# Kernel tuning notes

Measured on AMD Instinct MI355X. Metric: run time of the kernel, lower is better.

Reference implementation:

```python
import jax, jax.numpy as jnp
import numpy as np
from jax import lax

# Dims
HID = 2048          # hidden_size
DI = 4096           # d_inner = expand * hidden
NH = 64             # mamba heads
P = 64              # head dim
N = 128             # d_state
G = 1               # n_groups
K = 4               # conv kernel
IM = 8192           # MLP intermediate
BB, L = 2, 2048
EPS = 1e-5
CONV_DIM = DI + 2 * G * N            # 4352
D_IN_PROJ = 2 * DI + 2 * G * N + NH  # 8512


def rmsnorm(x, w, eps=EPS):
    v = jnp.mean(jnp.square(x), axis=-1, keepdims=True)
    return x * jax.lax.rsqrt(v + eps) * w


def setup_inputs() -> dict:
    key = jax.random.key(0)
    ks = jax.random.split(key, 16)
    s = 0.02
    return {
        "positions": jnp.broadcast_to(jnp.arange(L, dtype=jnp.int32), (BB, L)),
        "hidden_states": jax.random.normal(ks[0], (BB, L, HID), jnp.float32),
        "residual": jax.random.normal(ks[1], (BB, L, HID), jnp.float32),
        "in_proj_w": jax.random.normal(ks[2], (D_IN_PROJ, HID), jnp.float32) * s,
        "conv_w": jax.random.normal(ks[3], (CONV_DIM, K), jnp.float32) * 0.2,
        "conv_b": jax.random.normal(ks[4], (CONV_DIM,), jnp.float32) * 0.02,
        "A_log": jnp.log(jnp.arange(1, NH + 1, dtype=jnp.float32)),
        "D": jnp.ones((NH,), jnp.float32),
        "dt_bias": jax.random.uniform(ks[5], (NH,), jnp.float32, -4.0, -2.0),
        "mixer_norm_w": jnp.ones((DI,), jnp.float32),
        "out_proj_w": jax.random.normal(ks[6], (HID, DI), jnp.float32) * s,
        "input_ln_w": jnp.ones((HID,), jnp.float32),
        "pre_ff_ln_w": jnp.ones((HID,), jnp.float32),
        "gate_up_w": jax.random.normal(ks[7], (2 * IM, HID), jnp.float32) * s,
        "down_w": jax.random.normal(ks[8], (HID, IM), jnp.float32) * s,
    }


def reference(positions, hidden_states, residual, in_proj_w, conv_w, conv_b,
              A_log, D, dt_bias, mixer_norm_w, out_proj_w, input_ln_w,
              pre_ff_ln_w, gate_up_w, down_w):
    del positions  # not used by the mamba mixer math
    B_, Lq, _ = hidden_states.shape

    # --- input RMSNorm with fused residual add ---
    residual = hidden_states + residual
    hs = rmsnorm(residual, input_ln_w)

    # --- Mamba2 mixer ---
    proj = jnp.einsum('bld,ed->ble', hs, in_proj_w)   # [B,L,D_IN_PROJ]
    z = proj[..., :DI]
    xBC = proj[..., DI:DI + CONV_DIM]
    dt = proj[..., DI + CONV_DIM:]                    # [B,L,NH]

    # causal depthwise conv (kernel K) + SiLU
    xp = jnp.pad(xBC, ((0, 0), (K - 1, 0), (0, 0)))
    conv = conv_b
    for k in range(K):
        conv = conv + xp[:, k:k + Lq, :] * conv_w[:, k]
    xBC = jax.nn.silu(conv)

    x = xBC[..., :DI].reshape(B_, Lq, NH, P)
    Bm = xBC[..., DI:DI + G * N].reshape(B_, Lq, G, N)
    Cm = xBC[..., DI + G * N:].reshape(B_, Lq, G, N)
    rep = NH // G
    Bm = jnp.repeat(Bm, rep, axis=2)                  # [B,L,NH,N]
    Cm = jnp.repeat(Cm, rep, axis=2)

    dt = jax.nn.softplus(dt + dt_bias)                # [B,L,NH]
    A = -jnp.exp(A_log)                               # [NH]
    dA = jnp.exp(dt * A)                              # [B,L,NH]

    def step(h, inp):
        x_t, B_t, C_t, dA_t, dt_t = inp               # [B,NH,P],[B,NH,N],[B,NH,N],[B,NH],[B,NH]
        h = dA_t[..., None, None] * h + \
            (dt_t[..., None, None] * x_t[..., None]) * B_t[:, :, None, :]
        y = jnp.einsum('bhpn,bhn->bhp', h, C_t)
        return h, y

    xs = (x.transpose(1, 0, 2, 3), Bm.transpose(1, 0, 2, 3),
          Cm.transpose(1, 0, 2, 3), dA.transpose(1, 0, 2), dt.transpose(1, 0, 2))
    h0 = jnp.zeros((B_, NH, P, N), hidden_states.dtype)
    _, ys = lax.scan(step, h0, xs)                    # [L,B,NH,P]
    y = ys.transpose(1, 0, 2, 3) + D[None, None, :, None] * x
    y = y.reshape(B_, Lq, DI)

    # gated RMSNorm (Mixer2RMSNormGated, n_groups=1)
    y = y * jax.nn.silu(z)
    y = rmsnorm(y, mixer_norm_w)
    mamba_out = jnp.einsum('bld,hd->blh', y, out_proj_w)

    # --- pre-FF RMSNorm with fused residual add ---
    residual2 = mamba_out + residual
    hs2 = rmsnorm(residual2, pre_ff_ln_w)

    # --- gated MLP (SiluAndMul) ---
    gu = jnp.einsum('bld,ed->ble', hs2, gate_up_w)    # [B,L,2*IM]
    act = jax.nn.silu(gu[..., :IM]) * gu[..., IM:]
    out = jnp.einsum('bli,hi->blh', act, down_w)
    return out, residual2
```

## Files before the change

### kernel.cpp

```cpp
#include <hip/hip_runtime.h>

#define T_TOK 4096
#define HID   2048
#define DI    4096
#define NH    64
#define PDIM  64
#define NSTATE 128
#define IM    8192
#define LSEQ  2048
#define CONVD 4352
#define DPROJ 8512
#define DPADR 8704
#define QC    64
#define NCH   32

typedef __bf16 bf16x8 __attribute__((ext_vector_type(8)));
typedef float  f32x4  __attribute__((ext_vector_type(4)));

__device__ __forceinline__ unsigned short f2bf(float f) {
  unsigned u = __float_as_uint(f);
  u = (u + 0x7fffu + ((u >> 16) & 1u)) >> 16;
  return (unsigned short)u;
}
__device__ __forceinline__ float bf2f(unsigned short h) {
  return __uint_as_float(((unsigned)h) << 16);
}
__device__ __forceinline__ float siluf(float x) {
  return x / (1.f + __expf(-x));
}

#define GLL(gaddr, laddr) __builtin_amdgcn_global_load_lds( \
    (const __attribute__((address_space(1))) void*)(gaddr), \
    (__attribute__((address_space(3))) void*)(laddr), 16, 0, 0)

__global__ __launch_bounds__(256) void k_cvt(const float* __restrict__ src,
                                             unsigned short* __restrict__ dst, int n4) {
  int gid = blockIdx.x * 256 + threadIdx.x;
  if (gid >= n4) return;
  float4 v = *(const float4*)&src[(size_t)gid * 4];
  unsigned short* o = dst + (size_t)gid * 4;
  o[0] = f2bf(v.x); o[1] = f2bf(v.y); o[2] = f2bf(v.z); o[3] = f2bf(v.w);
}

__global__ __launch_bounds__(256) void k_cvt_inproj(const float* __restrict__ src,
                                                    unsigned short* __restrict__ dst) {
  int gid = blockIdx.x * 256 + threadIdx.x;
  size_t idx4 = (size_t)gid * 4;
  int r = (int)(idx4 >> 11);
  unsigned short* o = dst + idx4;
  if (r < DPROJ) {
    float4 v = *(const float4*)&src[(size_t)r * HID + (idx4 & 2047)];
    o[0] = f2bf(v.x); o[1] = f2bf(v.y); o[2] = f2bf(v.z); o[3] = f2bf(v.w);
  } else {
    o[0] = 0; o[1] = 0; o[2] = 0; o[3] = 0;
  }
}

__global__ __launch_bounds__(256) void k_cvt_gu(const float* __restrict__ src,
                                                unsigned short* __restrict__ dst) {
  int gid = blockIdx.x * 256 + threadIdx.x;
  size_t idx4 = (size_t)gid * 4;
  int r = (int)(idx4 >> 11), k = (int)(idx4 & 2047);
  int g = r >> 6, j = r & 63;
  int srcr = (j < 32) ? (g * 32 + j) : (IM + g * 32 + (j - 32));
  float4 v = *(const float4*)&src[(size_t)srcr * HID + k];
  unsigned short* o = dst + idx4;
  o[0] = f2bf(v.x); o[1] = f2bf(v.y); o[2] = f2bf(v.z); o[3] = f2bf(v.w);
}

template <int EPI>
__global__ __launch_bounds__(512, 2)
void gemm8(const unsigned short* __restrict__ A, const unsigned short* __restrict__ W,
           int K, int ntn, int ldo, void* __restrict__ outp,
           const float* __restrict__ resid) {
  __shared__ __align__(16) char smem[131072];
  const int t = threadIdx.x;
  const int w = t >> 6, l = t & 63;
  const int lr = l & 15, hi = l >> 4;
  const int wr = w >> 2, wc = w & 3;

  const int q = (int)gridDim.x >> 3;
  const int bid = blockIdx.x;
  const int id2 = (bid & 7) * q + (bid >> 3);
  const int tn = id2 >> 4, tm = id2 & 15;
  const int m0b = tm << 8, n0b = tn << 8;

  const int srow = t >> 3;
  const int scole = ((t & 7) << 3) ^ ((t & 32) ? 16 : 0) ^ ((t & 64) ? 32 : 0);
  const unsigned short* Ag = A + (size_t)(m0b + srow) * K + scole;
  const unsigned short* Wg = W + (size_t)(n0b + srow) * K + scole;
  const int ldsw = w * 1024;

  const int fa = ((lr & 4) ? 32 : 0) | ((lr & 8) ? 64 : 0);
  const int arow = (wr * 128 + lr) * 128 + hi * 16;
  const int brow = (wc * 64 + lr) * 128 + hi * 16;
  const int aoffk[2] = {arow ^ fa, (arow + 64) ^ fa};
  const int boffk[2] = {brow ^ fa, (brow + 64) ^ fa};

#define ISSUE_A(jt, hh, bb) do { int p_ = (hh) * 2;                                   \
    GLL(Ag + (size_t)(p_ * 64) * K + (jt) * 64,                                       \
        smem + (bb) * 65536 + p_ * 8192 + ldsw);                                      \
    GLL(Ag + (size_t)(p_ * 64 + 64) * K + (jt) * 64,                                  \
        smem + (bb) * 65536 + p_ * 8192 + 8192 + ldsw); } while (0)
#define ISSUE_B(jt, hh, bb) do { int p_ = (hh) * 2;                                   \
    GLL(Wg + (size_t)(p_ * 64) * K + (jt) * 64,                                       \
        smem + (bb) * 65536 + 32768 + p_ * 8192 + ldsw);                              \
    GLL(Wg + (size_t)(p_ * 64 + 64) * K + (jt) * 64,                                  \
        smem + (bb) * 65536 + 32768 + p_ * 8192 + 8192 + ldsw); } while (0)

  f32x4 acc[8][4];
#pragma unroll
  for (int m = 0; m < 8; m++)
#pragma unroll
    for (int n = 0; n < 4; n++) acc[m][n] = (f32x4){0.f, 0.f, 0.f, 0.f};

  const int nkt = K >> 6;
  ISSUE_A(0, 0, 0); ISSUE_A(0, 1, 0);
  ISSUE_B(0, 0, 0); ISSUE_B(0, 1, 0);
  ISSUE_A(1, 0, 1); ISSUE_A(1, 1, 1);
  asm volatile("s_waitcnt vmcnt(4)" ::: "memory");
  __builtin_amdgcn_s_barrier();

#define CLUSTER(m0_) do {                                                             \
    __builtin_amdgcn_s_setprio(1);                                                    \
    _Pragma("unroll")                                                                 \
    for (int m = m0_; m < m0_ + 2; m++)                                               \
      _Pragma("unroll")                                                               \
      for (int n = 0; n < 4; n++)                                                     \
        _Pragma("unroll")                                                             \
        for (int kk = 0; kk < 2; kk++)                                                \
          acc[m][n] = __builtin_amdgcn_mfma_f32_16x16x32_bf16(afr[m][kk], bfr[n][kk], \
                                                              acc[m][n], 0, 0, 0);    \
    __builtin_amdgcn_s_setprio(0); } while (0)

  for (int j = 0; j < nkt; ++j) {
    const int cur = j & 1, nxt = cur ^ 1;
    const char* Ab = smem + cur * 65536;
    const char* Bb = Ab + 32768;
    if (j + 1 < nkt) { ISSUE_B(j + 1, 0, nxt); ISSUE_B(j + 1, 1, nxt); }
    bf16x8 bfr[4][2], afr[8][2];
#pragma unroll
    for (int n = 0; n < 4; n++)
#pragma unroll
      for (int kk = 0; kk < 2; kk++)
        bfr[n][kk] = *(const bf16x8*)(Bb + boffk[kk] + n * 2048);
#pragma unroll
    for (int m = 0; m < 8; m++)
#pragma unroll
      for (int kk = 0; kk < 2; kk++)
        afr[m][kk] = *(const bf16x8*)(Ab + aoffk[kk] + m * 2048);
    __builtin_amdgcn_s_barrier();
    CLUSTER(0);
    __builtin_amdgcn_s_barrier();
    if (j + 2 < nkt) ISSUE_A(j + 2, 0, cur);
    CLUSTER(2);
    __builtin_amdgcn_s_barrier();
    if (j + 2 < nkt) ISSUE_A(j + 2, 1, cur);
    CLUSTER(4);
    __builtin_amdgcn_s_barrier();
    CLUSTER(6);
    if (j + 2 < nkt) { asm volatile("s_waitcnt vmcnt(4)" ::: "memory"); }
    else             { asm volatile("s_waitcnt vmcnt(0)" ::: "memory"); }
    __builtin_amdgcn_s_barrier();
  }

  if constexpr (EPI == 0) {
    unsigned short* op = (unsigned short*)outp;
#pragma unroll
    for (int m = 0; m < 8; m++)
#pragma unroll
      for (int n = 0; n < 4; n++)
#pragma unroll
        for (int r = 0; r < 4; r++) {
          int row = m0b + wr * 128 + m * 16 + hi * 4 + r;
          int col = n0b + wc * 64 + n * 16 + lr;
          op[(size_t)row * ldo + col] = f2bf(acc[m][n][r]);
        }
  } else if constexpr (EPI == 2) {
    unsigned short* op = (unsigned short*)outp;
    const int gbase = (n0b + wc * 64) >> 1;
#pragma unroll
    for (int m = 0; m < 8; m++)
#pragma unroll
      for (int n = 0; n < 2; n++)
#pragma unroll
        for (int r = 0; r < 4; r++) {
          int row = m0b + wr * 128 + m * 16 + hi * 4 + r;
          int col = gbase + n * 16 + lr;
          float g = acc[m][n][r], u = acc[m][n + 2][r];
          op[(size_t)row * ldo + col] = f2bf(siluf(g) * u);
        }
  } else {
    float* op = (float*)outp;
#pragma unroll
    for (int m = 0; m < 8; m++)
#pragma unroll
      for (int n = 0; n < 4; n++)
#pragma unroll
        for (int r = 0; r < 4; r++) {
          int row = m0b + wr * 128 + m * 16 + hi * 4 + r;
          int col = n0b + wc * 64 + n * 16 + lr;
          float v = acc[m][n][r];
          if constexpr (EPI == 1) v += resid[(size_t)row * ldo + col];
          op[(size_t)row * ldo + col] = v;
        }
  }
#undef ISSUE_A
#undef ISSUE_B
#undef CLUSTER
}

__device__ __forceinline__ float block_reduce_sum256(float v, float* sred) {
#pragma unroll
  for (int m = 32; m; m >>= 1) v += __shfl_xor(v, m);
  int t = threadIdx.x;
  if ((t & 63) == 0) sred[t >> 6] = v;
  __syncthreads();
  return sred[0] + sred[1] + sred[2] + sred[3];
}

__global__ __launch_bounds__(256)
void k_addnorm(const float* __restrict__ hin, const float* __restrict__ rin,
               const float* __restrict__ wln, float* __restrict__ rout,
               unsigned short* __restrict__ hbf) {
  __shared__ float sred[4];
  const int tok = blockIdx.x, t = threadIdx.x;
  const size_t base = (size_t)tok * HID + t * 8;
  float4 a0 = *(const float4*)&hin[base];
  float4 a1 = *(const float4*)&hin[base + 4];
  float4 b0 = *(const float4*)&rin[base];
  float4 b1 = *(const float4*)&rin[base + 4];
  float v[8] = {a0.x + b0.x, a0.y + b0.y, a0.z + b0.z, a0.w + b0.w,
                a1.x + b1.x, a1.y + b1.y, a1.z + b1.z, a1.w + b1.w};
  float ss = 0.f;
#pragma unroll
  for (int j = 0; j < 8; j++) ss += v[j] * v[j];
  float tot = block_reduce_sum256(ss, sred);
  float rms = rsqrtf(tot * (1.f / HID) + 1e-5f);
  *(float4*)&rout[base] = (float4){v[0], v[1], v[2], v[3]};
  *(float4*)&rout[base + 4] = (float4){v[4], v[5], v[6], v[7]};
  float4 w0 = *(const float4*)&wln[t * 8];
  float4 w1 = *(const float4*)&wln[t * 8 + 4];
  float wa[8] = {w0.x, w0.y, w0.z, w0.w, w1.x, w1.y, w1.z, w1.w};
  unsigned short o[8];
#pragma unroll
  for (int j = 0; j < 8; j++) o[j] = f2bf(v[j] * rms * wa[j]);
  *(ushort4*)&hbf[base] = *(ushort4*)&o[0];
  *(ushort4*)&hbf[base + 4] = *(ushort4*)&o[4];
}

__global__ __launch_bounds__(256)
void k_rmsnorm_bf(const float* __restrict__ src, const float* __restrict__ wln,
                  unsigned short* __restrict__ dst) {
  __shared__ float sred[4];
  const int tok = blockIdx.x, t = threadIdx.x;
  const size_t base = (size_t)tok * HID + t * 8;
  float4 a0 = *(const float4*)&src[base];
  float4 a1 = *(const float4*)&src[base + 4];
  float v[8] = {a0.x, a0.y, a0.z, a0.w, a1.x, a1.y, a1.z, a1.w};
  float ss = 0.f;
#pragma unroll
  for (int j = 0; j < 8; j++) ss += v[j] * v[j];
  float tot = block_reduce_sum256(ss, sred);
  float rms = rsqrtf(tot * (1.f / HID) + 1e-5f);
  float4 w0 = *(const float4*)&wln[t * 8];
  float4 w1 = *(const float4*)&wln[t * 8 + 4];
  float wa[8] = {w0.x, w0.y, w0.z, w0.w, w1.x, w1.y, w1.z, w1.w};
  unsigned short o[8];
#pragma unroll
  for (int j = 0; j < 8; j++) o[j] = f2bf(v[j] * rms * wa[j]);
  *(ushort4*)&dst[base] = *(ushort4*)&o[0];
  *(ushort4*)&dst[base + 4] = *(ushort4*)&o[4];
}

__global__ __launch_bounds__(256)
void k_gatenorm(const unsigned short* __restrict__ ybuf, const unsigned short* __restrict__ projbf,
                const float* __restrict__ wmix, unsigned short* __restrict__ ynorm) {
  __shared__ float sred[4];
  const int tok = blockIdx.x, t = threadIdx.x;
  const size_t yb = (size_t)tok * DI;
  const size_t pb = (size_t)tok * DPADR;
  float g[16];
  float ss = 0.f;
#pragma unroll
  for (int j = 0; j < 16; j++) {
    int idx = j * 256 + t;
    float yv = bf2f(ybuf[yb + idx]);
    float z = bf2f(projbf[pb + idx]);
    float gg = yv * siluf(z);
    g[j] = gg;
    ss += gg * gg;
  }
  float tot = block_reduce_sum256(ss, sred);
  float rms = rsqrtf(tot * (1.f / DI) + 1e-5f);
#pragma unroll
  for (int j = 0; j < 16; j++) {
    int idx = j * 256 + t;
    ynorm[yb + idx] = f2bf(g[j] * rms * wmix[idx]);
  }
}

__global__ __launch_bounds__(256)
void k_conv(const unsigned short* __restrict__ projbf, const float* __restrict__ cw,
            const float* __restrict__ cb, unsigned short* __restrict__ xbf,
            unsigned short* __restrict__ bcbf) {
  const int c = blockIdx.x * 256 + threadIdx.x;
  const int tk = blockIdx.y;
  const int lpos = tk & (LSEQ - 1);
  float4 wv = *(const float4*)&cw[c * 4];
  float wk[4] = {wv.x, wv.y, wv.z, wv.w};
  float acc = cb[c];
#pragma unroll
  for (int k = 0; k < 4; k++) {
    int lp = lpos - 3 + k;
    if (lp >= 0) acc += bf2f(projbf[(size_t)(tk - 3 + k) * DPADR + DI + c]) * wk[k];
  }
  unsigned short r = f2bf(siluf(acc));
  if (c < DI) xbf[(size_t)tk * DI + c] = r;
  else        bcbf[(size_t)tk * 256 + (c - DI)] = r;
}

__global__ __launch_bounds__(256)
void k_dt(const unsigned short* __restrict__ projbf, const float* __restrict__ dt_bias,
          float* __restrict__ dtg) {
  int gid = blockIdx.x * 256 + threadIdx.x;
  int tk = gid >> 6, hh = gid & 63;
  float x = bf2f(projbf[(size_t)tk * DPADR + (DI + CONVD) + hh]) + dt_bias[hh];
  float dt = (x > 20.f) ? x : log1pf(__expf(x));
  dtg[gid] = dt;
}

__global__ __launch_bounds__(256)
void k_ssd1(const unsigned short* __restrict__ xbf, const unsigned short* __restrict__ bcbf,
            const float* __restrict__ dtg, const float* __restrict__ A_log,
            const float* __restrict__ Dv, unsigned short* __restrict__ ybuf,
            unsigned short* __restrict__ Sc, float* __restrict__ dtsum) {
  __shared__ __align__(16) char smem[60928];
  unsigned short* sBs  = (unsigned short*)(smem);
  unsigned short* sCs  = (unsigned short*)(smem + 16384);
  unsigned short* sMs  = (unsigned short*)(smem + 16384);
  unsigned short* sBsT = (unsigned short*)(smem + 32768);
  unsigned short* sXsT = (unsigned short*)(smem + 51200);
  float* sdt = (float*)(smem + 60416);
  float* sdl = (float*)(smem + 60672);

  const int bi = blockIdx.x;
  const int ch = bi & 31, h = (bi >> 5) & 63, b = bi >> 11;
  const int bh = b * NH + h;
  const int tok0 = b * LSEQ + ch * QC;
  const int t = threadIdx.x;
  const int w = t >> 6, l = t & 63, lr = l & 15, hi = l >> 4;
  const float Ah = -__expf(A_log[h]);
  const float Dh = Dv[h];

  {
    const int srow = t >> 4, scol = (t & 15) * 8;
#pragma unroll
    for (int i = 0; i < 4; i++) {
      const unsigned short* gb = bcbf + (size_t)(tok0 + srow + 16 * i) * 256 + scol;
      GLL(gb, (char*)sBs + i * 4096 + w * 1024);
      GLL(gb + 128, (char*)sCs + i * 4096 + w * 1024);
    }
  }
  if (t < QC) sdt[t] = dtg[(size_t)(tok0 + t) * NH + h];
  __syncthreads();
  if (t < QC) sdl[t] = sdt[t];
  __syncthreads();
  for (int off = 1; off < QC; off <<= 1) {
    float v = 0.f;
    if (t < QC && t >= off) v = sdl[t - off];
    __syncthreads();
    if (t < QC) sdl[t] += v;
    __syncthreads();
  }

  {
    const int s = t >> 2;
    const float DlQ = sdl[QC - 1];
    const float csc = __expf(Ah * (DlQ - sdl[s])) * sdt[s];
    const int n0 = (t & 3) * 32;
#pragma unroll
    for (int j = 0; j < 32; j++) {
      float bv = bf2f(sBs[s * 128 + n0 + j]);
      sBsT[(n0 + j) * 72 + s] = f2bf(csc * bv);
    }
    const int p0 = (t & 3) * 16;
    const unsigned short* gx = xbf + (size_t)(tok0 + s) * DI + h * 64 + p0;
    union { uint4 v; unsigned short u[8]; } x0, x1;
    x0.v = *(const uint4*)gx;
    x1.v = *(const uint4*)(gx + 8);
#pragma unroll
    for (int j = 0; j < 8; j++) {
      sXsT[(p0 + j) * 72 + s] = x0.u[j];
      sXsT[(p0 + 8 + j) * 72 + s] = x1.u[j];
    }
  }
  __syncthreads();

  f32x4 accS[4];
#pragma unroll
  for (int jf = 0; jf < 4; jf++) accS[jf] = (f32x4){0.f, 0.f, 0.f, 0.f};
#pragma unroll
  for (int ks = 0; ks < 4; ks++) {
    bf16x8 a = *(const bf16x8*)&sBs[(w * 16 + lr) * 128 + ks * 32 + hi * 8];
#pragma unroll
    for (int jf = 0; jf < 4; jf++) {
      bf16x8 bb = *(const bf16x8*)&sCs[(jf * 16 + lr) * 128 + ks * 32 + hi * 8];
      accS[jf] = __builtin_amdgcn_mfma_f32_16x16x32_bf16(a, bb, accS[jf], 0, 0, 0);
    }
  }
  __syncthreads();

  {
    const int s0 = w * 16 + hi * 4;
#pragma unroll
    for (int jf = 0; jf < 4; jf++) {
      const int tt = jf * 16 + lr;
      const float dlt = sdl[tt];
      unsigned short mv[4];
#pragma unroll
      for (int r = 0; r < 4; r++) {
        const int ss = s0 + r;
        float val = 0.f;
        if (ss <= tt) val = accS[jf][r] * __expf(Ah * (dlt - sdl[ss])) * sdt[ss];
        mv[r] = f2bf(val);
      }
      *(ushort4*)&sMs[tt * 72 + s0] = *(ushort4*)mv;
    }
  }
  __syncthreads();

  {
    f32x4 accY[4];
#pragma unroll
    for (int jf = 0; jf < 4; jf++) accY[jf] = (f32x4){0.f, 0.f, 0.f, 0.f};
#pragma unroll
    for (int ks = 0; ks < 2; ks++) {
      bf16x8 a = *(const bf16x8*)&sMs[(w * 16 + lr) * 72 + ks * 32 + hi * 8];
#pragma unroll
      for (int jf = 0; jf < 4; jf++) {
        bf16x8 bb = *(const bf16x8*)&sXsT[(jf * 16 + lr) * 72 + ks * 32 + hi * 8];
        accY[jf] = __builtin_amdgcn_mfma_f32_16x16x32_bf16(a, bb, accY[jf], 0, 0, 0);
      }
    }
#pragma unroll
    for (int jf = 0; jf < 4; jf++)
#pragma unroll
      for (int r = 0; r < 4; r++) {
        const int tt = w * 16 + hi * 4 + r;
        const int pp = jf * 16 + lr;
        float xv = bf2f(sXsT[pp * 72 + tt]);
        ybuf[(size_t)(tok0 + tt) * DI + h * 64 + pp] = f2bf(accY[jf][r] + Dh * xv);
      }
  }

  {
    f32x4 accT[8];
#pragma unroll
    for (int jf = 0; jf < 8; jf++) accT[jf] = (f32x4){0.f, 0.f, 0.f, 0.f};
#pragma unroll
    for (int ks = 0; ks < 2; ks++) {
      bf16x8 a = *(const bf16x8*)&sXsT[(w * 16 + lr) * 72 + ks * 32 + hi * 8];
#pragma unroll
      for (int jf = 0; jf < 8; jf++) {
        bf16x8 bb = *(const bf16x8*)&sBsT[(jf * 16 + lr) * 72 + ks * 32 + hi * 8];
        accT[jf] = __builtin_amdgcn_mfma_f32_16x16x32_bf16(a, bb, accT[jf], 0, 0, 0);
      }
    }
    unsigned short* sc = Sc + ((size_t)bh * NCH + ch) * (PDIM * NSTATE);
#pragma unroll
    for (int jf = 0; jf < 8; jf++)
#pragma unroll
      for (int r = 0; r < 4; r++) {
        const int pp = w * 16 + hi * 4 + r;
        const int nn = jf * 16 + lr;
        sc[pp * NSTATE + nn] = f2bf(accT[jf][r]);
      }
  }
  if (t == 0) dtsum[bh * NCH + ch] = sdl[QC - 1];
}

__global__ __launch_bounds__(256)
void k_ssd2(const float* __restrict__ A_log, const float* __restrict__ dtsum,
            unsigned short* __restrict__ ScHt) {
  const int blk = blockIdx.x;
  const int bh = blk >> 3, pg = blk & 7;
  const int t = threadIdx.x;
  const int p = pg * 8 + (t >> 5), n0 = (t & 31) * 4;
  const int h = bh & 63;
  const float Ah = -__expf(A_log[h]);
  float H[4] = {0.f, 0.f, 0.f, 0.f};
  for (int c = 0; c < NCH; c++) {
    size_t base = (((size_t)bh * NCH + c) * PDIM + p) * NSTATE + n0;
    ushort4 sv = *(const ushort4*)&ScHt[base];
    float dec = __expf(Ah * dtsum[bh * NCH + c]);
    ushort4 hv;
    hv.x = f2bf(H[0]); hv.y = f2bf(H[1]); hv.z = f2bf(H[2]); hv.w = f2bf(H[3]);
    *(ushort4*)&ScHt[base] = hv;
    H[0] = dec * H[0] + bf2f(sv.x);
    H[1] = dec * H[1] + bf2f(sv.y);
    H[2] = dec * H[2] + bf2f(sv.z);
    H[3] = dec * H[3] + bf2f(sv.w);
  }
}

__global__ __launch_bounds__(256)
void k_ssd3(const unsigned short* __restrict__ bcbf, const unsigned short* __restrict__ Ht,
            const float* __restrict__ dtg, const float* __restrict__ A_log,
            unsigned short* __restrict__ ybuf) {
  __shared__ __align__(16) char smem[33280];
  unsigned short* sCs = (unsigned short*)(smem);
  unsigned short* sHt = (unsigned short*)(smem + 16384);
  float* sdt = (float*)(smem + 32768);
  float* sdl = (float*)(smem + 33024);

  const int bi = blockIdx.x;
  const int ch = bi & 31, h = (bi >> 5) & 63, b = bi >> 11;
  const int bh = b * NH + h;
  const int tok0 = b * LSEQ + ch * QC;
  const int t = threadIdx.x;
  const int w = t >> 6, l = t & 63, lr = l & 15, hi = l >> 4;
  const float Ah = -__expf(A_log[h]);

  {
    const int srow = t >> 4, scol = (t & 15) * 8;
    const unsigned short* gh = Ht + ((size_t)bh * NCH + ch) * (PDIM * NSTATE);
#pragma unroll
    for (int i = 0; i < 4; i++) {
      const unsigned short* gc = bcbf + (size_t)(tok0 + srow + 16 * i) * 256 + 128 + scol;
      GLL(gc, (char*)sCs + i * 4096 + w * 1024);
      GLL(gh + i * 2048 + t * 8, (char*)sHt + i * 4096 + w * 1024);
    }
  }
  if (t < QC) sdt[t] = dtg[(size_t)(tok0 + t) * NH + h];
  __syncthreads();
  if (t < QC) sdl[t] = sdt[t];
  __syncthreads();
  for (int off = 1; off < QC; off <<= 1) {
    float v = 0.f;
    if (t < QC && t >= off) v = sdl[t - off];
    __syncthreads();
    if (t < QC) sdl[t] += v;
    __syncthreads();
  }

  f32x4 acc[4];
#pragma unroll
  for (int jf = 0; jf < 4; jf++) acc[jf] = (f32x4){0.f, 0.f, 0.f, 0.f};
#pragma unroll
  for (int ks = 0; ks < 4; ks++) {
    bf16x8 a = *(const bf16x8*)&sCs[(w * 16 + lr) * 128 + ks * 32 + hi * 8];
#pragma unroll
    for (int jf = 0; jf < 4; jf++) {
      bf16x8 bb = *(const bf16x8*)&sHt[(jf * 16 + lr) * 128 + ks * 32 + hi * 8];
      acc[jf] = __builtin_amdgcn_mfma_f32_16x16x32_bf16(a, bb, acc[jf], 0, 0, 0);
    }
  }
#pragma unroll
  for (int jf = 0; jf < 4; jf++)
#pragma unroll
    for (int r = 0; r < 4; r++) {
      const int tt = w * 16 + hi * 4 + r;
      const int pp = jf * 16 + lr;
      const float dec = __expf(Ah * sdl[tt]);
      const size_t o = (size_t)(tok0 + tt) * DI + h * 64 + pp;
      ybuf[o] = f2bf(bf2f(ybuf[o]) + dec * acc[jf][r]);
    }
}

static const size_t OFF_WBF_IN  = 0;
static const size_t OFF_WBF_OUT = 35651584;
static const size_t OFF_WBF_GU  = 52428800;
static const size_t OFF_WBF_DN  = 119537664;
static const size_t OFF_RESID   = 153092096;
static const size_t OFF_HSBF    = 186646528;
static const size_t OFF_PROJ    = 203423744;
static const size_t OFF_XBF     = 274726912;
static const size_t OFF_BCBF    = 308281344;
static const size_t OFF_DTG     = 310378496;
static const size_t OFF_YBUF    = 311427072;
static const size_t OFF_SC      = 344981504;
static const size_t OFF_DTSUM   = 412090368;

extern "C" void kernel_launch(void* const* d_in, const int* in_sizes, int n_in,
                              void* d_out, int out_size, void* d_ws, size_t ws_size,
                              hipStream_t stream) {
  (void)in_sizes; (void)n_in; (void)out_size; (void)ws_size;
  const float* hidden   = (const float*)d_in[1];
  const float* resin    = (const float*)d_in[2];
  const float* w_inproj = (const float*)d_in[3];
  const float* conv_w   = (const float*)d_in[4];
  const float* conv_b   = (const float*)d_in[5];
  const float* A_log    = (const float*)d_in[6];
  const float* Dvec     = (const float*)d_in[7];
  const float* dt_bias  = (const float*)d_in[8];
  const float* w_mix    = (const float*)d_in[9];
  const float* w_outp   = (const float*)d_in[10];
  const float* w_ln1    = (const float*)d_in[11];
  const float* w_ln2    = (const float*)d_in[12];
  const float* w_gu     = (const float*)d_in[13];
  const float* w_dn     = (const float*)d_in[14];

  char* ws = (char*)d_ws;
  unsigned short* wbf_in  = (unsigned short*)(ws + OFF_WBF_IN);
  unsigned short* wbf_out = (unsigned short*)(ws + OFF_WBF_OUT);
  unsigned short* wbf_gu  = (unsigned short*)(ws + OFF_WBF_GU);
  unsigned short* wbf_dn  = (unsigned short*)(ws + OFF_WBF_DN);
  float*          residb  = (float*)(ws + OFF_RESID);
  unsigned short* hsbf    = (unsigned short*)(ws + OFF_HSBF);
  unsigned short* projbf  = (unsigned short*)(ws + OFF_PROJ);
  unsigned short* actbf   = (unsigned short*)(ws + OFF_PROJ);
  unsigned short* xbf     = (unsigned short*)(ws + OFF_XBF);
  unsigned short* ynormbf = (unsigned short*)(ws + OFF_XBF);
  unsigned short* bcbf    = (unsigned short*)(ws + OFF_BCBF);
  float*          dtgb    = (float*)(ws + OFF_DTG);
  unsigned short* ybuf    = (unsigned short*)(ws + OFF_YBUF);
  unsigned short* scht    = (unsigned short*)(ws + OFF_SC);
  float*          dtsumb  = (float*)(ws + OFF_DTSUM);

  float* out0 = (float*)d_out;
  float* res2 = out0 + (size_t)T_TOK * HID;

  k_cvt_inproj<<<17408, 256, 0, stream>>>(w_inproj, wbf_in);
  k_cvt<<<8192, 256, 0, stream>>>(w_outp, wbf_out, 2097152);
  k_cvt_gu<<<32768, 256, 0, stream>>>(w_gu, wbf_gu);
  k_cvt<<<16384, 256, 0, stream>>>(w_dn, wbf_dn, 4194304);

  k_addnorm<<<T_TOK, 256, 0, stream>>>(hidden, resin, w_ln1, residb, hsbf);
  gemm8<0><<<34 * 16, 512, 0, stream>>>(hsbf, wbf_in, HID, 34, DPADR, projbf, nullptr);
  k_conv<<<dim3(17, T_TOK), 256, 0, stream>>>(projbf, conv_w, conv_b, xbf, bcbf);
  k_dt<<<T_TOK * NH / 256, 256, 0, stream>>>(projbf, dt_bias, dtgb);
  k_ssd1<<<4096, 256, 0, stream>>>(xbf, bcbf, dtgb, A_log, Dvec, ybuf, scht, dtsumb);
  k_ssd2<<<1024, 256, 0, stream>>>(A_log, dtsumb, scht);
  k_ssd3<<<4096, 256, 0, stream>>>(bcbf, scht, dtgb, A_log, ybuf);
  k_gatenorm<<<T_TOK, 256, 0, stream>>>(ybuf, projbf, w_mix, ynormbf);
  gemm8<1><<<8 * 16, 512, 0, stream>>>(ynormbf, wbf_out, DI, 8, HID, res2, residb);
  k_rmsnorm_bf<<<T_TOK, 256, 0, stream>>>(res2, w_ln2, hsbf);
  gemm8<2><<<64 * 16, 512, 0, stream>>>(hsbf, wbf_gu, HID, 64, IM, actbf, nullptr);
  gemm8<3><<<8 * 16, 512, 0, stream>>>(actbf, wbf_dn, IM, 8, HID, out0, nullptr);
}
```

Measured before the change: 1.195 ms.

## Template GEMM on M-tile size and simplify double-buffered pipeline

Adds a BM template parameter so the N=2048 GEMMs (out_proj and down_proj) use 128-row tiles, doubling their grid from 128 to 256 blocks to fill more CUs. The main loop changes from a split A/B prefetch schedule with partial vmcnt waits and several barriers to a plain double buffer: wait for all loads, one barrier, issue the next tile, then interleave LDS fragment reads with MFMA groups. This trades some latency hiding and per-block reuse for better occupancy on the small-N GEMMs. It also changes the large GEMMs' scheduling.

```diff
diff --git a/kernel.cpp b/kernel.cpp
--- a/kernel.cpp
+++ b/kernel.cpp
@@ -68,12 +68,17 @@
   o[0] = f2bf(v.x); o[1] = f2bf(v.y); o[2] = f2bf(v.z); o[3] = f2bf(v.w);
 }
 
-template <int EPI>
+template <int EPI, int BM>
 __global__ __launch_bounds__(512, 2)
 void gemm8(const unsigned short* __restrict__ A, const unsigned short* __restrict__ W,
            int K, int ntn, int ldo, void* __restrict__ outp,
            const float* __restrict__ resid) {
-  __shared__ __align__(16) char smem[131072];
+  (void)ntn;
+  constexpr int MREP  = BM / 32;
+  constexpr int ABYT  = BM * 128;
+  constexpr int BUFB  = ABYT + 32768;
+  constexpr int NTM   = 4096 / BM;
+  __shared__ __align__(16) char smem[2 * BUFB];
   const int t = threadIdx.x;
   const int w = t >> 6, l = t & 63;
   const int lr = l & 15, hi = l >> 4;
@@ -82,8 +87,8 @@
   const int q = (int)gridDim.x >> 3;
   const int bid = blockIdx.x;
   const int id2 = (bid & 7) * q + (bid >> 3);
-  const int tn = id2 >> 4, tm = id2 & 15;
-  const int m0b = tm << 8, n0b = tn << 8;
+  const int tn = id2 / NTM, tm = id2 % NTM;
+  const int m0b = tm * BM, n0b = tn << 8;
 
   const int srow = t >> 3;
   const int scole = ((t & 7) << 3) ^ ((t & 32) ? 16 : 0) ^ ((t & 64) ? 32 : 0);
@@ -92,87 +97,96 @@
   const int ldsw = w * 1024;
 
   const int fa = ((lr & 4) ? 32 : 0) | ((lr & 8) ? 64 : 0);
-  const int arow = (wr * 128 + lr) * 128 + hi * 16;
+  const int arow = (wr * (BM / 2) + lr) * 128 + hi * 16;
   const int brow = (wc * 64 + lr) * 128 + hi * 16;
-  const int aoffk[2] = {arow ^ fa, (arow + 64) ^ fa};
-  const int boffk[2] = {brow ^ fa, (brow + 64) ^ fa};
-
-#define ISSUE_A(jt, hh, bb) do { int p_ = (hh) * 2;                                   \
-    GLL(Ag + (size_t)(p_ * 64) * K + (jt) * 64,                                       \
-        smem + (bb) * 65536 + p_ * 8192 + ldsw);                                      \
-    GLL(Ag + (size_t)(p_ * 64 + 64) * K + (jt) * 64,                                  \
-        smem + (bb) * 65536 + p_ * 8192 + 8192 + ldsw); } while (0)
-#define ISSUE_B(jt, hh, bb) do { int p_ = (hh) * 2;                                   \
-    GLL(Wg + (size_t)(p_ * 64) * K + (jt) * 64,                                       \
-        smem + (bb) * 65536 + 32768 + p_ * 8192 + ldsw);                              \
-    GLL(Wg + (size_t)(p_ * 64 + 64) * K + (jt) * 64,                                  \
-        smem + (bb) * 65536 + 32768 + p_ * 8192 + 8192 + ldsw); } while (0)
-
-  f32x4 acc[8][4];
-#pragma unroll
-  for (int m = 0; m < 8; m++)
+  const int aoff0 = arow ^ fa, aoff1 = (arow + 64) ^ fa;
+  const int boff0 = brow ^ fa, boff1 = (brow + 64) ^ fa;
+
+#define ISSUE_A(jt, bb) do {                                                    \
+    _Pragma("unroll")                                                           \
+    for (int p_ = 0; p_ < BM / 64; ++p_)                                        \
+      GLL(Ag + (size_t)(p_ * 64) * K + (size_t)(jt) * 64,                       \
+          smem + (bb) * BUFB + p_ * 8192 + ldsw); } while (0)
+#define ISSUE_B(jt, bb) do {                                                    \
+    _Pragma("unroll")                                                           \
+    for (int p_ = 0; p_ < 4; ++p_)                                              \
+      GLL(Wg + (size_t)(p_ * 64) * K + (size_t)(jt) * 64,                       \
+          smem + (bb) * BUFB + ABYT + p_ * 8192 + ldsw); } while (0)
+
+#define RDF(off, base) (*(const bf16x8*)((base) + (off)))
+#define MF(P, x, y, c0, c1, c2, c3) do {                                                     \
+    __builtin_amdgcn_s_setprio(1);                                                           \
+    acc[2*(P)  ][0] = __builtin_amdgcn_mfma_f32_16x16x32_bf16((x),(c0),acc[2*(P)  ][0],0,0,0);\
+    acc[2*(P)+1][0] = __builtin_amdgcn_mfma_f32_16x16x32_bf16((y),(c0),acc[2*(P)+1][0],0,0,0);\
+    acc[2*(P)  ][1] = __builtin_amdgcn_mfma_f32_16x16x32_bf16((x),(c1),acc[2*(P)  ][1],0,0,0);\
+    acc[2*(P)+1][1] = __builtin_amdgcn_mfma_f32_16x16x32_bf16((y),(c1),acc[2*(P)+1][1],0,0,0);\
+    acc[2*(P)  ][2] = __builtin_amdgcn_mfma_f32_16x16x32_bf16((x),(c2),acc[2*(P)  ][2],0,0,0);\
+    acc[2*(P)+1][2] = __builtin_amdgcn_mfma_f32_16x16x32_bf16((y),(c2),acc[2*(P)+1][2],0,0,0);\
+    acc[2*(P)  ][3] = __builtin_amdgcn_mfma_f32_16x16x32_bf16((x),(c3),acc[2*(P)  ][3],0,0,0);\
+    acc[2*(P)+1][3] = __builtin_amdgcn_mfma_f32_16x16x32_bf16((y),(c3),acc[2*(P)+1][3],0,0,0);\
+    __builtin_amdgcn_s_setprio(0); } while (0)
+
+  f32x4 acc[MREP][4];
+#pragma unroll
+  for (int m = 0; m < MREP; m++)
 #pragma unroll
     for (int n = 0; n < 4; n++) acc[m][n] = (f32x4){0.f, 0.f, 0.f, 0.f};
 
   const int nkt = K >> 6;
-  ISSUE_A(0, 0, 0); ISSUE_A(0, 1, 0);
-  ISSUE_B(0, 0, 0); ISSUE_B(0, 1, 0);
-  ISSUE_A(1, 0, 1); ISSUE_A(1, 1, 1);
-  asm volatile("s_waitcnt vmcnt(4)" ::: "memory");
-  __builtin_amdgcn_s_barrier();
-
-#define CLUSTER(m0_) do {                                                             \
-    __builtin_amdgcn_s_setprio(1);                                                    \
-    _Pragma("unroll")                                                                 \
-    for (int m = m0_; m < m0_ + 2; m++)                                               \
-      _Pragma("unroll")                                                               \
-      for (int n = 0; n < 4; n++)                                                     \
-        _Pragma("unroll")                                                             \
-        for (int kk = 0; kk < 2; kk++)                                                \
-          acc[m][n] = __builtin_amdgcn_mfma_f32_16x16x32_bf16(afr[m][kk], bfr[n][kk], \
-                                                              acc[m][n], 0, 0, 0);    \
-    __builtin_amdgcn_s_setprio(0); } while (0)
+  ISSUE_A(0, 0); ISSUE_B(0, 0);
 
   for (int j = 0; j < nkt; ++j) {
-    const int cur = j & 1, nxt = cur ^ 1;
-    const char* Ab = smem + cur * 65536;
-    const char* Bb = Ab + 32768;
-    if (j + 1 < nkt) { ISSUE_B(j + 1, 0, nxt); ISSUE_B(j + 1, 1, nxt); }
-    bf16x8 bfr[4][2], afr[8][2];
-#pragma unroll
-    for (int n = 0; n < 4; n++)
-#pragma unroll
-      for (int kk = 0; kk < 2; kk++)
-        bfr[n][kk] = *(const bf16x8*)(Bb + boffk[kk] + n * 2048);
-#pragma unroll
-    for (int m = 0; m < 8; m++)
-#pragma unroll
-      for (int kk = 0; kk < 2; kk++)
-        afr[m][kk] = *(const bf16x8*)(Ab + aoffk[kk] + m * 2048);
+    const int cur = j & 1;
+    const char* Ab = smem + cur * BUFB;
+    const char* Bb = Ab + ABYT;
+    asm volatile("s_waitcnt vmcnt(0)" ::: "memory");
     __builtin_amdgcn_s_barrier();
-    CLUSTER(0);
-    __builtin_amdgcn_s_barrier();
-    if (j + 2 < nkt) ISSUE_A(j + 2, 0, cur);
-    CLUSTER(2);
-    __builtin_amdgcn_s_barrier();
-    if (j + 2 < nkt) ISSUE_A(j + 2, 1, cur);
-    CLUSTER(4);
-    __builtin_amdgcn_s_barrier();
-    CLUSTER(6);
-    if (j + 2 < nkt) { asm volatile("s_waitcnt vmcnt(4)" ::: "memory"); }
-    else             { asm volatile("s_waitcnt vmcnt(0)" ::: "memory"); }
-    __builtin_amdgcn_s_barrier();
+    __builtin_amdgcn_sched_barrier(0);
+    if (j + 1 < nkt) { ISSUE_A(j + 1, cur ^ 1); ISSUE_B(j + 1, cur ^ 1); }
+    bf16x8 b0 = RDF(boff0, Bb), b1 = RDF(boff0 + 2048, Bb),
+           b2 = RDF(boff0 + 4096, Bb), b3 = RDF(boff0 + 6144, Bb);
+    bf16x8 af0 = RDF(aoff0, Ab), af1 = RDF(aoff0 + 2048, Ab);
+    bf16x8 af2, af3, b4, b5, b6, b7;
+    if constexpr (MREP == 8) {
+      af2 = RDF(aoff0 + 4096, Ab); af3 = RDF(aoff0 + 6144, Ab);
+      MF(0, af0, af1, b0, b1, b2, b3);
+      af0 = RDF(aoff0 + 8192, Ab); af1 = RDF(aoff0 + 10240, Ab);
+      MF(1, af2, af3, b0, b1, b2, b3);
+      af2 = RDF(aoff0 + 12288, Ab); af3 = RDF(aoff0 + 14336, Ab);
+      MF(2, af0, af1, b0, b1, b2, b3);
+      b4 = RDF(boff1, Bb); b5 = RDF(boff1 + 2048, Bb);
+      b6 = RDF(boff1 + 4096, Bb); b7 = RDF(boff1 + 6144, Bb);
+      af0 = RDF(aoff1, Ab); af1 = RDF(aoff1 + 2048, Ab);
+      MF(3, af2, af3, b0, b1, b2, b3);
+      af2 = RDF(aoff1 + 4096, Ab); af3 = RDF(aoff1 + 6144, Ab);
+      MF(0, af0, af1, b4, b5, b6, b7);
+      af0 = RDF(aoff1 + 8192, Ab); af1 = RDF(aoff1 + 10240, Ab);
+      MF(1, af2, af3, b4, b5, b6, b7);
+      af2 = RDF(aoff1 + 12288, Ab); af3 = RDF(aoff1 + 14336, Ab);
+      MF(2, af0, af1, b4, b5, b6, b7);
+      MF(3, af2, af3, b4, b5, b6, b7);
+    } else {
+      af2 = RDF(aoff0 + 4096, Ab); af3 = RDF(aoff0 + 6144, Ab);
+      MF(0, af0, af1, b0, b1, b2, b3);
+      b4 = RDF(boff1, Bb); b5 = RDF(boff1 + 2048, Bb);
+      b6 = RDF(boff1 + 4096, Bb); b7 = RDF(boff1 + 6144, Bb);
+      af0 = RDF(aoff1, Ab); af1 = RDF(aoff1 + 2048, Ab);
+      MF(1, af2, af3, b0, b1, b2, b3);
+      af2 = RDF(aoff1 + 4096, Ab); af3 = RDF(aoff1 + 6144, Ab);
+      MF(0, af0, af1, b4, b5, b6, b7);
+      MF(1, af2, af3, b4, b5, b6, b7);
+    }
   }
 
   if constexpr (EPI == 0) {
     unsigned short* op = (unsigned short*)outp;
 #pragma unroll
-    for (int m = 0; m < 8; m++)
+    for (int m = 0; m < MREP; m++)
 #pragma unroll
       for (int n = 0; n < 4; n++)
 #pragma unroll
         for (int r = 0; r < 4; r++) {
-          int row = m0b + wr * 128 + m * 16 + hi * 4 + r;
+          int row = m0b + wr * (BM / 2) + m * 16 + hi * 4 + r;
           int col = n0b + wc * 64 + n * 16 + lr;
           op[(size_t)row * ldo + col] = f2bf(acc[m][n][r]);
         }
@@ -180,12 +194,12 @@
     unsigned short* op = (unsigned short*)outp;
     const int gbase = (n0b + wc * 64) >> 1;
 #pragma unroll
-    for (int m = 0; m < 8; m++)
+    for (int m = 0; m < MREP; m++)
 #pragma unroll
       for (int n = 0; n < 2; n++)
 #pragma unroll
         for (int r = 0; r < 4; r++) {
-          int row = m0b + wr * 128 + m * 16 + hi * 4 + r;
+          int row = m0b + wr * (BM / 2) + m * 16 + hi * 4 + r;
           int col = gbase + n * 16 + lr;
           float g = acc[m][n][r], u = acc[m][n + 2][r];
           op[(size_t)row * ldo + col] = f2bf(siluf(g) * u);
@@ -193,12 +207,12 @@
   } else {
     float* op = (float*)outp;
 #pragma unroll
-    for (int m = 0; m < 8; m++)
+    for (int m = 0; m < MREP; m++)
 #pragma unroll
       for (int n = 0; n < 4; n++)
 #pragma unroll
         for (int r = 0; r < 4; r++) {
-          int row = m0b + wr * 128 + m * 16 + hi * 4 + r;
+          int row = m0b + wr * (BM / 2) + m * 16 + hi * 4 + r;
           int col = n0b + wc * 64 + n * 16 + lr;
           float v = acc[m][n][r];
           if constexpr (EPI == 1) v += resid[(size_t)row * ldo + col];
@@ -207,7 +221,8 @@
   }
 #undef ISSUE_A
 #undef ISSUE_B
-#undef CLUSTER
+#undef RDF
+#undef MF
 }
 
 __device__ __forceinline__ float block_reduce_sum256(float v, float* sred) {
@@ -627,15 +642,15 @@
   k_cvt<<<16384, 256, 0, stream>>>(w_dn, wbf_dn, 4194304);
 
   k_addnorm<<<T_TOK, 256, 0, stream>>>(hidden, resin, w_ln1, residb, hsbf);
-  gemm8<0><<<34 * 16, 512, 0, stream>>>(hsbf, wbf_in, HID, 34, DPADR, projbf, nullptr);
+  gemm8<0, 256><<<34 * 16, 512, 0, stream>>>(hsbf, wbf_in, HID, 34, DPADR, projbf, nullptr);
   k_conv<<<dim3(17, T_TOK), 256, 0, stream>>>(projbf, conv_w, conv_b, xbf, bcbf);
   k_dt<<<T_TOK * NH / 256, 256, 0, stream>>>(projbf, dt_bias, dtgb);
   k_ssd1<<<4096, 256, 0, stream>>>(xbf, bcbf, dtgb, A_log, Dvec, ybuf, scht, dtsumb);
   k_ssd2<<<1024, 256, 0, stream>>>(A_log, dtsumb, scht);
   k_ssd3<<<4096, 256, 0, stream>>>(bcbf, scht, dtgb, A_log, ybuf);
   k_gatenorm<<<T_TOK, 256, 0, stream>>>(ybuf, projbf, w_mix, ynormbf);
-  gemm8<1><<<8 * 16, 512, 0, stream>>>(ynormbf, wbf_out, DI, 8, HID, res2, residb);
+  gemm8<1, 128><<<8 * 32, 512, 0, stream>>>(ynormbf, wbf_out, DI, 8, HID, res2, residb);
   k_rmsnorm_bf<<<T_TOK, 256, 0, stream>>>(res2, w_ln2, hsbf);
-  gemm8<2><<<64 * 16, 512, 0, stream>>>(hsbf, wbf_gu, HID, 64, IM, actbf, nullptr);
-  gemm8<3><<<8 * 16, 512, 0, stream>>>(actbf, wbf_dn, IM, 8, HID, out0, nullptr);
-}
+  gemm8<2, 256><<<64 * 16, 512, 0, stream>>>(hsbf, wbf_gu, HID, 64, IM, actbf, nullptr);
+  gemm8<3, 128><<<8 * 32, 512, 0, stream>>>(actbf, wbf_dn, IM, 8, HID, out0, nullptr);
+}
```

After: 1.007 ms. -15.8%, faster.
